# Kernel optimization log

Hardware: AMD Instinct MI355X
Metric: run time of the kernel (lower is better)

Reference implementation:

```python
import jax, jax.numpy as jnp
import numpy as np

LN_EPS = 1e-5

def setup_inputs() -> dict:
    key = jax.random.key(0)
    ks = jax.random.split(key, 4)
    B, T, D = 8, 2048, 1024
    x = jax.random.normal(ks[0], (B, T, D), dtype=jnp.float32)
    Wz = jax.random.normal(ks[1], (D, D), dtype=jnp.float32) * (1.0 / np.sqrt(D))
    bz = jnp.zeros((D,), dtype=jnp.float32)
    Wh = jax.random.normal(ks[2], (D, D), dtype=jnp.float32) * (1.0 / np.sqrt(D))
    bh = jnp.zeros((D,), dtype=jnp.float32)
    swish_beta = jnp.float32(1.0)
    ln_gamma = jnp.ones((D,), dtype=jnp.float32)
    ln_beta = jnp.zeros((D,), dtype=jnp.float32)
    return {"x": x, "Wz": Wz, "bz": bz, "Wh": Wh, "bh": bh,
            "swish_beta": swish_beta, "ln_gamma": ln_gamma, "ln_beta": ln_beta}

def _min_gru(x, Wz, bz, Wh, bh):
    # x: [B,T,D]. minGRU: h_t = (1-z_t)*h_{t-1} + z_t*h_tilde_t, h_0 = 0.
    z = jax.nn.sigmoid(jnp.einsum('btd,de->bte', x, Wz) + bz)   # [B,T,D]
    h_tilde = jnp.einsum('btd,de->bte', x, Wh) + bh             # [B,T,D]
    a = 1.0 - z
    b = z * h_tilde
    # parallel associative scan over time for h_t = a_t*h_{t-1} + b_t
    def combine(c1, c2):
        a1, b1 = c1
        a2, b2 = c2
        return a1 * a2, a2 * b1 + b2
    _, h = jax.lax.associative_scan(combine, (a, b), axis=1)
    return h  # [B,T,D]

def reference(x, Wz, bz, Wh, bh, swish_beta, ln_gamma, ln_beta):
    h = _min_gru(x, Wz, bz, Wh, bh)
    # Swish with learnable beta: silu(beta*x) = (beta*x)*sigmoid(beta*x)
    s = swish_beta * h
    y = s * jax.nn.sigmoid(s)
    # LayerNorm over last dim (channels_last)
    mu = jnp.mean(y, axis=-1, keepdims=True)
    var = jnp.mean(jnp.square(y - mu), axis=-1, keepdims=True)
    out = (y - mu) * jax.lax.rsqrt(var + LN_EPS) * ln_gamma + ln_beta
    return out
```

## Files before the change

### kernel.cpp

```cpp
#include <hip/hip_runtime.h>

#define GLOBAL_AS __attribute__((address_space(1)))
#define LDS_AS __attribute__((address_space(3)))

typedef unsigned short u16;
typedef unsigned int u32;
typedef __bf16 bf16x8 __attribute__((ext_vector_type(8)));
typedef float f32x4 __attribute__((ext_vector_type(4)));

static constexpr int BB = 8;
static constexpr int TT = 2048;
static constexpr int DD = 1024;
static constexpr int MM = BB * TT;
static constexpr int KK = DD;
static constexpr int NC = 64;
static constexpr int CL = TT / NC;
static constexpr int NCH = BB * NC;

__device__ __forceinline__ u16 f2bf(float f) {
  union { float f; u32 u; } c; c.f = f;
  u32 u = c.u;
  u32 r = (u + 0x7fffu + ((u >> 16) & 1u)) >> 16;
  return (u16)r;
}

__global__ void cvt_x_kernel(const float* __restrict__ x, u16* __restrict__ xb) {
  int i = (blockIdx.x * blockDim.x + threadIdx.x) * 8;
  const float4* p = reinterpret_cast<const float4*>(x + i);
  float4 v0 = p[0], v1 = p[1];
  u16 r0 = f2bf(v0.x), r1 = f2bf(v0.y), r2 = f2bf(v0.z), r3 = f2bf(v0.w);
  u16 r4 = f2bf(v1.x), r5 = f2bf(v1.y), r6 = f2bf(v1.z), r7 = f2bf(v1.w);
  uint4 o;
  o.x = (u32)r0 | ((u32)r1 << 16);
  o.y = (u32)r2 | ((u32)r3 << 16);
  o.z = (u32)r4 | ((u32)r5 << 16);
  o.w = (u32)r6 | ((u32)r7 << 16);
  *reinterpret_cast<uint4*>(xb + i) = o;
}

__global__ void cvt_w_kernel(const float* __restrict__ Wz, const float* __restrict__ Wh,
                             u16* __restrict__ WT) {
  __shared__ float tile[32][33];
  int w = blockIdx.z;
  const float* W = w ? Wh : Wz;
  u16* O = WT + (size_t)w * DD * KK;
  int k0 = blockIdx.y * 32;
  int n0 = blockIdx.x * 32;
  int tx = threadIdx.x, ty = threadIdx.y;
  for (int i = 0; i < 32; i += 8)
    tile[ty + i][tx] = W[(size_t)(k0 + ty + i) * DD + n0 + tx];
  __syncthreads();
  for (int i = 0; i < 32; i += 8)
    O[(size_t)(n0 + ty + i) * KK + k0 + tx] = f2bf(tile[tx][ty + i]);
}

__global__ __launch_bounds__(256) void gemm_dual_kernel(
    const u16* __restrict__ xb,
    const u16* __restrict__ WT,
    const float* __restrict__ bz, const float* __restrict__ bh,
    float* __restrict__ a_out, float* __restrict__ bb_out,
    float* __restrict__ Asum, float* __restrict__ Bsum) {
  __shared__ __align__(16) u16 As[128 * 32];
  __shared__ __align__(16) u16 Bzs[64 * 32];
  __shared__ __align__(16) u16 Bhs[64 * 32];

  int bid = blockIdx.x;
  int nt = bid & 15;
  int mt = bid >> 4;
  int m0 = mt * 128, n0 = nt * 64;

  int tid = threadIdx.x;
  int lane = tid & 63;
  int wave = tid >> 6;

  int drow = tid >> 2;
  int dk = (tid & 3) * 8;
  const u16* Ag0 = xb + (size_t)(m0 + drow) * KK + dk;
  const u16* Ag1 = Ag0 + (size_t)64 * KK;
  const u16* Bzg = WT + (size_t)(n0 + drow) * KK + dk;
  const u16* Bhg = Bzg + (size_t)DD * KK;

  u16* As0W = As + wave * 512;
  u16* As1W = As + 2048 + wave * 512;
  u16* BzsW = Bzs + wave * 512;
  u16* BhsW = Bhs + wave * 512;

  f32x4 accz[2][4];
  f32x4 acch[2][4];
  for (int i = 0; i < 2; i++)
    for (int j = 0; j < 4; j++) {
      accz[i][j] = (f32x4){0.f, 0.f, 0.f, 0.f};
      acch[i][j] = (f32x4){0.f, 0.f, 0.f, 0.f};
    }

  int RM = wave * 32;
  int fr = lane & 15;
  int fk = (lane >> 4) * 8;

  for (int k0i = 0; k0i < KK; k0i += 32) {
    __builtin_amdgcn_global_load_lds((const GLOBAL_AS void*)(Ag0 + k0i), (LDS_AS void*)As0W, 16, 0, 0);
    __builtin_amdgcn_global_load_lds((const GLOBAL_AS void*)(Ag1 + k0i), (LDS_AS void*)As1W, 16, 0, 0);
    __builtin_amdgcn_global_load_lds((const GLOBAL_AS void*)(Bzg + k0i), (LDS_AS void*)BzsW, 16, 0, 0);
    __builtin_amdgcn_global_load_lds((const GLOBAL_AS void*)(Bhg + k0i), (LDS_AS void*)BhsW, 16, 0, 0);
    __syncthreads();

    bf16x8 af[2], bzf[4], bhf[4];
    for (int i = 0; i < 2; i++)
      af[i] = *reinterpret_cast<const bf16x8*>(As + (RM + i * 16 + fr) * 32 + fk);
    for (int j = 0; j < 4; j++) {
      bzf[j] = *reinterpret_cast<const bf16x8*>(Bzs + (j * 16 + fr) * 32 + fk);
      bhf[j] = *reinterpret_cast<const bf16x8*>(Bhs + (j * 16 + fr) * 32 + fk);
    }
    for (int i = 0; i < 2; i++)
      for (int j = 0; j < 4; j++) {
        accz[i][j] = __builtin_amdgcn_mfma_f32_16x16x32_bf16(af[i], bzf[j], accz[i][j], 0, 0, 0);
        acch[i][j] = __builtin_amdgcn_mfma_f32_16x16x32_bf16(af[i], bhf[j], acch[i][j], 0, 0, 0);
      }
    __syncthreads();
  }

  int quad = lane >> 4;
  int cg = mt * 4 + wave;
  for (int j = 0; j < 4; j++) {
    int n = n0 + j * 16 + fr;
    float bzv = bz[n], bhv = bh[n];
    float Ai[2], Bi[2];
    for (int i = 0; i < 2; i++) {
      float Aloc = 1.f, Bloc = 0.f;
      int mbase = m0 + RM + i * 16 + quad * 4;
      for (int r = 0; r < 4; r++) {
        float zp = accz[i][j][r] + bzv;
        float hp = acch[i][j][r] + bhv;
        float zs = 1.0f / (1.0f + __expf(-zp));
        float av = 1.0f - zs;
        float bv = zs * hp;
        size_t idx = (size_t)(mbase + r) * DD + n;
        a_out[idx] = av;
        bb_out[idx] = bv;
        Bloc = av * Bloc + bv;
        Aloc = av * Aloc;
      }
      {
        float Ao = __shfl_xor(Aloc, 16, 64);
        float Bo = __shfl_xor(Bloc, 16, 64);
        float Bc = (quad & 1) ? (Aloc * Bo + Bloc) : (Ao * Bloc + Bo);
        float Ac = Aloc * Ao;
        float Ao2 = __shfl_xor(Ac, 32, 64);
        float Bo2 = __shfl_xor(Bc, 32, 64);
        Bi[i] = (quad & 2) ? (Ac * Bo2 + Bc) : (Ao2 * Bc + Bo2);
        Ai[i] = Ac * Ao2;
      }
    }
    float Ack = Ai[1] * Ai[0];
    float Bck = Ai[1] * Bi[0] + Bi[1];
    if (quad == 0) {
      Asum[(size_t)cg * DD + n] = Ack;
      Bsum[(size_t)cg * DD + n] = Bck;
    }
  }
}

__global__ void chunk_scan_kernel(const float* __restrict__ Asum, const float* __restrict__ Bsum,
                                  float* __restrict__ hin) {
  int tid = blockIdx.x * blockDim.x + threadIdx.x;
  int d = tid & (DD - 1);
  int b = tid >> 10;
  float h = 0.f;
#pragma unroll
  for (int c = 0; c < NC; c++) {
    int i = (b * NC + c) * DD + d;
    hin[i] = h;
    h = Asum[i] * h + Bsum[i];
  }
}

__global__ __launch_bounds__(256) void apply_ln_kernel(
    const float* __restrict__ a, const float* __restrict__ bb, const float* __restrict__ hin,
    const float* __restrict__ sbeta, const float* __restrict__ gamma,
    const float* __restrict__ lbeta, float* __restrict__ out) {
  __shared__ float ps[2][4];
  __shared__ float pq[2][4];
  int ch = blockIdx.x;
  int wv = threadIdx.x >> 6;
  int lane = threadIdx.x & 63;
  int d = wv * 256 + lane * 4;
  int b = ch >> 6, c = ch & (NC - 1);
  float sb = sbeta[0];

  float4 g4 = *reinterpret_cast<const float4*>(gamma + d);
  float4 be4 = *reinterpret_cast<const float4*>(lbeta + d);
  float4 h4 = *reinterpret_cast<const float4*>(hin + (size_t)ch * DD + d);

  size_t base = ((size_t)b * TT + (size_t)c * CL) * DD + d;

  float4 aR[3], bR[3];
#pragma unroll
  for (int p = 0; p < 3; p++) {
    aR[p] = *reinterpret_cast<const float4*>(a + base + (size_t)p * DD);
    bR[p] = *reinterpret_cast<const float4*>(bb + base + (size_t)p * DD);
  }

#pragma unroll
  for (int t = 0; t < CL; t++) {
    const int slot = t % 3;
    const int pslot = t & 1;
    float4 av = aR[slot], bv = bR[slot];
    h4.x = av.x * h4.x + bv.x;
    h4.y = av.y * h4.y + bv.y;
    h4.z = av.z * h4.z + bv.z;
    h4.w = av.w * h4.w + bv.w;
    if (t + 3 < CL) {
      aR[slot] = *reinterpret_cast<const float4*>(a + base + (size_t)(t + 3) * DD);
      bR[slot] = *reinterpret_cast<const float4*>(bb + base + (size_t)(t + 3) * DD);
    }
    float sx = sb * h4.x, sy = sb * h4.y, sz = sb * h4.z, sw = sb * h4.w;
    float4 y;
    y.x = sx / (1.0f + __expf(-sx));
    y.y = sy / (1.0f + __expf(-sy));
    y.z = sz / (1.0f + __expf(-sz));
    y.w = sw / (1.0f + __expf(-sw));
    float sum = y.x + y.y + y.z + y.w;
    float sq = y.x * y.x + y.y * y.y + y.z * y.z + y.w * y.w;
#pragma unroll
    for (int o = 32; o > 0; o >>= 1) {
      sum += __shfl_xor(sum, o, 64);
      sq += __shfl_xor(sq, o, 64);
    }
    if (lane == 0) { ps[pslot][wv] = sum; pq[pslot][wv] = sq; }
    __syncthreads();
    float tot = ps[pslot][0] + ps[pslot][1] + ps[pslot][2] + ps[pslot][3];
    float totq = pq[pslot][0] + pq[pslot][1] + pq[pslot][2] + pq[pslot][3];
    float mu = tot * (1.0f / DD);
    float var = totq * (1.0f / DD) - mu * mu;
    float inv = rsqrtf(fmaxf(var, 0.f) + 1e-5f);
    float4 o4;
    o4.x = (y.x - mu) * inv * g4.x + be4.x;
    o4.y = (y.y - mu) * inv * g4.y + be4.y;
    o4.z = (y.z - mu) * inv * g4.z + be4.z;
    o4.w = (y.w - mu) * inv * g4.w + be4.w;
    *reinterpret_cast<float4*>(out + base + (size_t)t * DD) = o4;
  }
}

extern "C" void kernel_launch(void* const* d_in, const int* in_sizes, int n_in,
                              void* d_out, int out_size, void* d_ws, size_t ws_size,
                              hipStream_t stream) {
  const float* x     = (const float*)d_in[0];
  const float* Wz    = (const float*)d_in[1];
  const float* bz    = (const float*)d_in[2];
  const float* Wh    = (const float*)d_in[3];
  const float* bh    = (const float*)d_in[4];
  const float* sbeta = (const float*)d_in[5];
  const float* gamma = (const float*)d_in[6];
  const float* lbeta = (const float*)d_in[7];
  float* out = (float*)d_out;

  char* ws = (char*)d_ws;
  u16* xb     = (u16*)ws;
  u16* WT     = (u16*)(ws + 33554432);
  float* bb   = (float*)(ws + 37748736);
  float* Asum = (float*)(ws + 104857600);
  float* Bsum = (float*)(ws + 106954752);
  float* hin  = (float*)(ws + 109051904);
  const size_t NEED_BASE = 111149056ull;
  const size_t NEED_FULL = NEED_BASE + 67108864ull;
  float* a_ptr = (ws_size >= NEED_FULL) ? (float*)(ws + NEED_BASE) : out;

  cvt_x_kernel<<<8192, 256, 0, stream>>>(x, xb);
  dim3 tw(32, 8), gw(32, 32, 2);
  cvt_w_kernel<<<gw, tw, 0, stream>>>(Wz, Wh, WT);
  gemm_dual_kernel<<<2048, 256, 0, stream>>>(xb, WT, bz, bh, a_ptr, bb, Asum, Bsum);
  chunk_scan_kernel<<<32, 256, 0, stream>>>(Asum, Bsum, hin);
  apply_ln_kernel<<<NCH, 256, 0, stream>>>(a_ptr, bb, hin, sbeta, gamma, lbeta, out);
}
```

Measured before the change: 284.6 us.

## Split fused scan-swish-layernorm into per-column scan kernel and row layernorm kernel

Replaces the fused chunk apply kernel, which synchronized the block every timestep to reduce LayerNorm statistics, with two kernels. The first runs the intra-chunk scan per column with scalar threads and writes swish output in place over the a buffer. The second does a per-row LayerNorm with one wavefront per row and no block barriers. This removes per-step __syncthreads and raises parallelism, but adds a full extra write and read of the activation tensor.

```diff
diff --git a/kernel.cpp b/kernel.cpp
--- a/kernel.cpp
+++ b/kernel.cpp
@@ -174,71 +174,60 @@
   }
 }
 
-__global__ __launch_bounds__(256) void apply_ln_kernel(
-    const float* __restrict__ a, const float* __restrict__ bb, const float* __restrict__ hin,
-    const float* __restrict__ sbeta, const float* __restrict__ gamma,
-    const float* __restrict__ lbeta, float* __restrict__ out) {
-  __shared__ float ps[2][4];
-  __shared__ float pq[2][4];
-  int ch = blockIdx.x;
-  int wv = threadIdx.x >> 6;
-  int lane = threadIdx.x & 63;
-  int d = wv * 256 + lane * 4;
+__global__ __launch_bounds__(256) void apply_h_kernel(
+    float* __restrict__ a, const float* __restrict__ bb, const float* __restrict__ hin,
+    const float* __restrict__ sbeta) {
+  int tid = blockIdx.x * blockDim.x + threadIdx.x;
+  int d = tid & (DD - 1);
+  int ch = tid >> 10;
   int b = ch >> 6, c = ch & (NC - 1);
   float sb = sbeta[0];
-
-  float4 g4 = *reinterpret_cast<const float4*>(gamma + d);
-  float4 be4 = *reinterpret_cast<const float4*>(lbeta + d);
-  float4 h4 = *reinterpret_cast<const float4*>(hin + (size_t)ch * DD + d);
-
+  float h = hin[(size_t)ch * DD + d];
   size_t base = ((size_t)b * TT + (size_t)c * CL) * DD + d;
-
-  float4 aR[3], bR[3];
-#pragma unroll
-  for (int p = 0; p < 3; p++) {
-    aR[p] = *reinterpret_cast<const float4*>(a + base + (size_t)p * DD);
-    bR[p] = *reinterpret_cast<const float4*>(bb + base + (size_t)p * DD);
-  }
-
-#pragma unroll
+#pragma unroll 8
   for (int t = 0; t < CL; t++) {
-    const int slot = t % 3;
-    const int pslot = t & 1;
-    float4 av = aR[slot], bv = bR[slot];
-    h4.x = av.x * h4.x + bv.x;
-    h4.y = av.y * h4.y + bv.y;
-    h4.z = av.z * h4.z + bv.z;
-    h4.w = av.w * h4.w + bv.w;
-    if (t + 3 < CL) {
-      aR[slot] = *reinterpret_cast<const float4*>(a + base + (size_t)(t + 3) * DD);
-      bR[slot] = *reinterpret_cast<const float4*>(bb + base + (size_t)(t + 3) * DD);
-    }
-    float sx = sb * h4.x, sy = sb * h4.y, sz = sb * h4.z, sw = sb * h4.w;
-    float4 y;
-    y.x = sx / (1.0f + __expf(-sx));
-    y.y = sy / (1.0f + __expf(-sy));
-    y.z = sz / (1.0f + __expf(-sz));
-    y.w = sw / (1.0f + __expf(-sw));
-    float sum = y.x + y.y + y.z + y.w;
-    float sq = y.x * y.x + y.y * y.y + y.z * y.z + y.w * y.w;
-#pragma unroll
-    for (int o = 32; o > 0; o >>= 1) {
-      sum += __shfl_xor(sum, o, 64);
-      sq += __shfl_xor(sq, o, 64);
-    }
-    if (lane == 0) { ps[pslot][wv] = sum; pq[pslot][wv] = sq; }
-    __syncthreads();
-    float tot = ps[pslot][0] + ps[pslot][1] + ps[pslot][2] + ps[pslot][3];
-    float totq = pq[pslot][0] + pq[pslot][1] + pq[pslot][2] + pq[pslot][3];
-    float mu = tot * (1.0f / DD);
-    float var = totq * (1.0f / DD) - mu * mu;
-    float inv = rsqrtf(fmaxf(var, 0.f) + 1e-5f);
+    size_t idx = base + (size_t)t * DD;
+    float av = a[idx];
+    float bv = bb[idx];
+    h = av * h + bv;
+    float s = sb * h;
+    a[idx] = s / (1.0f + __expf(-s));
+  }
+}
+
+__global__ __launch_bounds__(256) void row_ln_kernel(
+    const float* __restrict__ y, const float* __restrict__ gamma,
+    const float* __restrict__ lbeta, float* __restrict__ out) {
+  int row = (blockIdx.x << 2) | (threadIdx.x >> 6);
+  int lane = threadIdx.x & 63;
+  size_t rb = (size_t)row * DD + lane * 4;
+
+  float4 v[4];
+  float sum = 0.f, sq = 0.f;
+#pragma unroll
+  for (int j = 0; j < 4; j++) {
+    v[j] = *reinterpret_cast<const float4*>(y + rb + j * 256);
+    sum += v[j].x + v[j].y + v[j].z + v[j].w;
+    sq += v[j].x * v[j].x + v[j].y * v[j].y + v[j].z * v[j].z + v[j].w * v[j].w;
+  }
+#pragma unroll
+  for (int o = 32; o > 0; o >>= 1) {
+    sum += __shfl_xor(sum, o, 64);
+    sq += __shfl_xor(sq, o, 64);
+  }
+  float mu = sum * (1.0f / DD);
+  float var = sq * (1.0f / DD) - mu * mu;
+  float inv = rsqrtf(fmaxf(var, 0.f) + 1e-5f);
+#pragma unroll
+  for (int j = 0; j < 4; j++) {
+    float4 g4 = *reinterpret_cast<const float4*>(gamma + lane * 4 + j * 256);
+    float4 be4 = *reinterpret_cast<const float4*>(lbeta + lane * 4 + j * 256);
     float4 o4;
-    o4.x = (y.x - mu) * inv * g4.x + be4.x;
-    o4.y = (y.y - mu) * inv * g4.y + be4.y;
-    o4.z = (y.z - mu) * inv * g4.z + be4.z;
-    o4.w = (y.w - mu) * inv * g4.w + be4.w;
-    *reinterpret_cast<float4*>(out + base + (size_t)t * DD) = o4;
+    o4.x = (v[j].x - mu) * inv * g4.x + be4.x;
+    o4.y = (v[j].y - mu) * inv * g4.y + be4.y;
+    o4.z = (v[j].z - mu) * inv * g4.z + be4.z;
+    o4.w = (v[j].w - mu) * inv * g4.w + be4.w;
+    *reinterpret_cast<float4*>(out + rb + j * 256) = o4;
   }
 }
 
@@ -271,5 +260,6 @@
   cvt_w_kernel<<<gw, tw, 0, stream>>>(Wz, Wh, WT);
   gemm_dual_kernel<<<2048, 256, 0, stream>>>(xb, WT, bz, bh, a_ptr, bb, Asum, Bsum);
   chunk_scan_kernel<<<32, 256, 0, stream>>>(Asum, Bsum, hin);
-  apply_ln_kernel<<<NCH, 256, 0, stream>>>(a_ptr, bb, hin, sbeta, gamma, lbeta, out);
-}
+  apply_h_kernel<<<2048, 256, 0, stream>>>(a_ptr, bb, hin, sbeta);
+  row_ln_kernel<<<4096, 256, 0, stream>>>(a_ptr, gamma, lbeta, out);
+}
```

Result: slower. 299.9 us (+5.4%).
